# Optimization experiments

Measured on AMD Instinct MI355X. Metric: run time of the kernel, lower is better.

The kernel has to match this reference:

```python
import jax, jax.numpy as jnp
import numpy as np
from jax import lax

# config: B=8, T=32, input_chans=1, H=kernel_size=8, W=n_freq=256
# F1=32, F2=48, F3=256, F4=128, n_note=88, pooling_size=2, filter_size3=(3,64)
B, T, CIN, H, W = 8, 32, 1, 8, 256
F1, F2, F3, F4, NNOTE = 32, 48, 256, 128, 88


def _conv2d(x, w, b, padding):
    # x: (B, Cin, H, W), w: (Cout, Cin, kh, kw)
    y = lax.conv_general_dilated(x, w, (1, 1), padding,
                                 dimension_numbers=('NCHW', 'OIHW', 'NCHW'))
    return y + b[None, :, None, None]


def _clstm(x, w, b, F):
    # x: (B, C, T, H, W); ConvLSTM (no peephole, no LN), 'same' padding.
    xs = jnp.moveaxis(x, 2, 0)  # (T, B, C, H, W)
    h0 = jnp.zeros((x.shape[0], F, x.shape[3], x.shape[4]), x.dtype)
    c0 = h0

    def step(carry, xt):
        h, c = carry
        z = _conv2d(jnp.concatenate([xt, h], axis=1), w, b, 'SAME')
        i, f, g, o = jnp.split(z, 4, axis=1)
        c = jax.nn.sigmoid(f) * c + jax.nn.sigmoid(i) * jnp.tanh(g)
        h = jax.nn.sigmoid(o) * jnp.tanh(c)
        return (h, c), h

    _, hs = lax.scan(step, (h0, c0), xs)  # (T, B, F, H, W)
    return jnp.moveaxis(hs, 0, 2)  # (B, F, T, H, W)


def _maxpool3d(x):
    # MaxPool3d(kernel=2, stride=2) over (T, H, W) of a (B, C, T, H, W) tensor
    return lax.reduce_window(x, -jnp.inf, lax.max,
                             (1, 1, 2, 2, 2), (1, 1, 2, 2, 2), 'VALID')


def setup_inputs() -> dict:
    key = jax.random.key(0)
    ks = jax.random.split(key, 11)
    s = 0.05
    return {
        'x':  jax.random.normal(ks[0], (B, CIN, T, H, W), jnp.float32),
        'w1': jax.random.normal(ks[1], (4 * F1, CIN + F1, 3, 3), jnp.float32) * s,
        'b1': jnp.zeros((4 * F1,), jnp.float32),
        'w2': jax.random.normal(ks[2], (4 * F2, F1 + F2, 3, 3), jnp.float32) * s,
        'b2': jnp.zeros((4 * F2,), jnp.float32),
        'w3': jax.random.normal(ks[3], (F3, F2, 3, 64), jnp.float32) * s,
        'b3': jnp.zeros((F3,), jnp.float32),
        'w4': jax.random.normal(ks[4], (F4, F3, 1, 1), jnp.float32) * s,
        'b4': jnp.zeros((F4,), jnp.float32),
        'w5': jax.random.normal(ks[5], (NNOTE, F4, 1, 1), jnp.float32) * s,
        'b5': jnp.zeros((NNOTE,), jnp.float32),
    }


def reference(x, w1, b1, w2, b2, w3, b3, w4, b4, w5, b5):
    x = _clstm(x, w1, b1, F1)          # (B, F1, T, H, W)
    x = _maxpool3d(x)                  # (B, F1, T/2, H/2, W/2)
    x = _clstm(x, w2, b2, F2)          # (B, F2, T/2, H/2, W/2)
    x = _maxpool3d(x)                  # (B, F2, 8, 2, 64)
    x = x.reshape(B, F2, -1, 64)       # (B, F2, 16, 64), filter_size3[1]=64
    x = jax.nn.elu(_conv2d(x, w3, b3, 'VALID'))  # (B, F3, 14, 1); dropout=eval noop
    x = jax.nn.elu(_conv2d(x, w4, b4, 'VALID'))  # (B, F4, 14, 1)
    x = _conv2d(x, w5, b5, 'VALID')              # (B, 88, 14, 1)
    return x
```

## Files before the change

kernel.cpp:

```cpp
#include <hip/hip_runtime.h>
#include <math.h>


#define DEVINL static __device__ __forceinline__
typedef __attribute__((ext_vector_type(8))) short short8;
typedef __attribute__((ext_vector_type(4))) float f32x4;

#define PLANE_W3 2359296

DEVINL float sigm(float x) { return 1.0f / (1.0f + __expf(-x)); }
DEVINL float tanh_fast(float x) { return 1.0f - 2.0f / (__expf(2.0f * x) + 1.0f); }
DEVINL float elu(float x) { return x > 0.0f ? x : expm1f(x); }
DEVINL unsigned short bf16_rne(float v) {
    unsigned u = __float_as_uint(v);
    unsigned r = (u + 0x7FFF + ((u >> 16) & 1)) >> 16;
    return (unsigned short)r;
}
DEVINL float bf16_to_f(unsigned short h) { return __uint_as_float(((unsigned)h) << 16); }
DEVINL unsigned pack_hl(float v) {
    unsigned short hi = bf16_rne(v);
    unsigned short lo = bf16_rne(v - bf16_to_f(hi));
    return (unsigned)hi | ((unsigned)lo << 16);
}
DEVINL float upk(unsigned u) {
    return __uint_as_float(u << 16) + __uint_as_float(u & 0xffff0000u);
}

DEVINL void lstm1_body(
    int xq, int y, int b, int t,
    const unsigned* __restrict__ xpk, const unsigned short* __restrict__ w1F,
    const float* __restrict__ b1,
    const unsigned* __restrict__ hprev, const unsigned* __restrict__ hpool,
    unsigned* __restrict__ hout, float* __restrict__ c1,
    unsigned* __restrict__ p1pk)
{
    __shared__ __align__(16) unsigned short sBhi[34 * 128];
    __shared__ __align__(16) unsigned short sBlo[34 * 128];
    const int x0 = xq * 32;
    const int tid = threadIdx.x;

    if (((t & 1) == 0) && t >= 2 && (y & 1) == 1) {
        int tp = (t >> 1) - 1, yp = y >> 1;
        for (int e = tid; e < 512; e += 256) {
            int f = e >> 4, xl = e & 15;
            int xp = (x0 >> 1) + xl, gx = x0 + 2 * xl;
            int b0 = ((b * 32 + f) * 8 + (y - 1)) * 256 + gx;
            float m = upk(hpool[b0]);
            m = fmaxf(m, upk(hpool[b0 + 1]));
            m = fmaxf(m, upk(hpool[b0 + 256]));
            m = fmaxf(m, upk(hpool[b0 + 257]));
            m = fmaxf(m, upk(hprev[b0]));
            m = fmaxf(m, upk(hprev[b0 + 1]));
            m = fmaxf(m, upk(hprev[b0 + 256]));
            m = fmaxf(m, upk(hprev[b0 + 257]));
            p1pk[(((b * 32 + f) * 16 + tp) * 4 + yp) * 128 + xp] = pack_hl(m);
        }
    }

    for (int e = tid; e < 34 * 128; e += 256) {
        int lx = e % 34, kk = e / 34;
        unsigned u = 0;
        if (kk < 99) {
            int ci = kk / 3, dy = kk - ci * 3;
            int gy = y + dy - 1, gx = x0 + lx - 1;
            if (gy >= 0 && gy < 8 && gx >= 0 && gx < 256)
                u = (ci == 0) ? xpk[((b * 32 + t) * 8 + gy) * 256 + gx]
                              : hprev[((b * 32 + (ci - 1)) * 8 + gy) * 256 + gx];
        }
        int a16 = lx * 128 + (((kk >> 3) ^ (lx & 15)) << 3) + (kk & 7);
        sBhi[a16] = (unsigned short)u;
        sBlo[a16] = (unsigned short)(u >> 16);
    }
    __syncthreads();

    const int l = tid & 63;
    const int wv = __builtin_amdgcn_readfirstlane(tid >> 6);
    const int ln = l & 15, kg = l >> 4;
    f32x4 acc[2][2];
#pragma unroll
    for (int i = 0; i < 2; ++i)
#pragma unroll
        for (int j = 0; j < 2; ++j) acc[i][j] = (f32x4){0.f, 0.f, 0.f, 0.f};

#pragma unroll
    for (int kk = 0; kk < 4; ++kk) {
        short8 bh[2][3], bl[2][3];
#pragma unroll
        for (int ntl = 0; ntl < 2; ++ntl)
#pragma unroll
            for (int dx = 0; dx < 3; ++dx) {
                int lx = ntl * 16 + ln + dx;
                int slot = kk * 4 + kg;
                int boff = lx * 128 + ((slot ^ (lx & 15)) << 3);
                bh[ntl][dx] = *(const short8*)&sBhi[boff];
                bl[ntl][dx] = *(const short8*)&sBlo[boff];
            }
#pragma unroll
        for (int mtl = 0; mtl < 2; ++mtl)
#pragma unroll
            for (int dx = 0; dx < 3; ++dx) {
                int aoff = ((((dx * 8 + wv * 2 + mtl) * 4 + kk) * 4 + kg) * 16 + ln) * 8;
                short8 ah = *(const short8*)&w1F[aoff];
#pragma unroll
                for (int ntl = 0; ntl < 2; ++ntl) {
                    acc[mtl][ntl] = __builtin_amdgcn_mfma_f32_16x16x32_bf16(ah, bl[ntl][dx], acc[mtl][ntl], 0, 0, 0);
                    acc[mtl][ntl] = __builtin_amdgcn_mfma_f32_16x16x32_bf16(ah, bh[ntl][dx], acc[mtl][ntl], 0, 0, 0);
                }
            }
    }

#pragma unroll
    for (int mtl = 0; mtl < 2; ++mtl) {
        const int f = (wv * 2 + mtl) * 4 + kg;
        const float bi = b1[f], bff = b1[32 + f], bg = b1[64 + f], bo = b1[96 + f];
#pragma unroll
        for (int ntl = 0; ntl < 2; ++ntl) {
            f32x4 a = acc[mtl][ntl];
            int gidx = ((b * 32 + f) * 8 + y) * 256 + x0 + ntl * 16 + ln;
            float zi = a[0] + bi, zf = a[1] + bff, zg = a[2] + bg, zo = a[3] + bo;
            float cv = c1[gidx];
            float cn = sigm(zf) * cv + sigm(zi) * tanh_fast(zg);
            c1[gidx] = cn;
            hout[gidx] = pack_hl(sigm(zo) * tanh_fast(cn));
        }
    }
}

DEVINL void lstm2_body(
    int xq, int y, int b, int t,
    const unsigned* __restrict__ p1pk, const unsigned short* __restrict__ w2F,
    const float* __restrict__ b2,
    const unsigned* __restrict__ hprev, const unsigned* __restrict__ hpool,
    float* __restrict__ c2, unsigned* __restrict__ hout,
    unsigned short* __restrict__ p2hi, unsigned short* __restrict__ p2lo)
{
    __shared__ __align__(16) unsigned short sChi[18 * 256];
    __shared__ __align__(16) unsigned short sClo[18 * 256];
    const int x0 = xq * 16;
    const int tid = threadIdx.x;

    if (((t & 1) == 0) && t >= 2 && y < 2) {
        int tp = (t >> 1) - 1;
        for (int e = tid; e < 48 * 8; e += 256) {
            int f = e >> 3, xl = e & 7;
            int xp = xq * 8 + xl;
            int g0 = ((b * 48 + f) * 4 + y * 2) * 128 + xp * 2;
            float m = fmaxf(fmaxf(upk(hpool[g0]), upk(hpool[g0 + 1])),
                            fmaxf(upk(hpool[g0 + 128]), upk(hpool[g0 + 129])));
            m = fmaxf(m, fmaxf(fmaxf(upk(hprev[g0]), upk(hprev[g0 + 1])),
                               fmaxf(upk(hprev[g0 + 128]), upk(hprev[g0 + 129]))));
            int pi = ((b * 48 + f) * 16 + tp * 2 + y) * 64 + xp;
            unsigned pm = pack_hl(m);
            p2hi[pi] = (unsigned short)pm;
            p2lo[pi] = (unsigned short)(pm >> 16);
        }
    }

    for (int idx = tid; idx < 80 * 54; idx += 256) {
        int ci = idx / 54, rem = idx % 54;
        int dy = rem / 18, lx = rem % 18;
        int gy = y + dy - 1, gx = x0 + lx - 1;
        unsigned u = 0;
        if (gy >= 0 && gy < 4 && gx >= 0 && gx < 128)
            u = (ci < 32) ? p1pk[(((b * 32 + ci) * 16 + t) * 4 + gy) * 128 + gx]
                          : hprev[((b * 48 + (ci - 32)) * 4 + gy) * 128 + gx];
        int k = ci * 3 + dy;
        int a16 = lx * 256 + (((k >> 3) ^ (lx & 15)) << 3) + (k & 7);
        sChi[a16] = (unsigned short)u;
        sClo[a16] = (unsigned short)(u >> 16);
    }
    for (int e = tid; e < 18 * 16; e += 256) {
        int lx = e >> 4, k = 240 + (e & 15);
        int a16 = lx * 256 + (((k >> 3) ^ (lx & 15)) << 3) + (k & 7);
        sChi[a16] = 0;
        sClo[a16] = 0;
    }
    __syncthreads();

    const int l = tid & 63;
    const int wv = __builtin_amdgcn_readfirstlane(tid >> 6);
    const int ln = l & 15, kg = l >> 4;
    f32x4 acc[3] = {{0.f,0.f,0.f,0.f},{0.f,0.f,0.f,0.f},{0.f,0.f,0.f,0.f}};

#pragma unroll
    for (int kk = 0; kk < 8; ++kk) {
        short8 bh[3], bl[3];
#pragma unroll
        for (int dx = 0; dx < 3; ++dx) {
            int lx = ln + dx;
            int boff = lx * 256 + ((((kk << 2) + kg) ^ (lx & 15)) << 3);
            bh[dx] = *(const short8*)&sChi[boff];
            bl[dx] = *(const short8*)&sClo[boff];
        }
#pragma unroll
        for (int j = 0; j < 3; ++j) {
            int mt = wv * 3 + j;
#pragma unroll
            for (int dx = 0; dx < 3; ++dx) {
                int aoff = ((((dx * 12 + mt) * 8 + kk) * 4 + kg) * 16 + ln) * 8;
                short8 ah = *(const short8*)&w2F[aoff];
                acc[j] = __builtin_amdgcn_mfma_f32_16x16x32_bf16(ah, bl[dx], acc[j], 0, 0, 0);
                acc[j] = __builtin_amdgcn_mfma_f32_16x16x32_bf16(ah, bh[dx], acc[j], 0, 0, 0);
            }
        }
    }

    const int x = x0 + ln;
#pragma unroll
    for (int j = 0; j < 3; ++j) {
        int mt = wv * 3 + j;
        int f = mt * 4 + kg;
        float zi = acc[j][0] + b2[f];
        float zf = acc[j][1] + b2[48 + f];
        float zg = acc[j][2] + b2[96 + f];
        float zo = acc[j][3] + b2[144 + f];
        int gidx = ((b * 48 + f) * 4 + y) * 128 + x;
        float cv = c2[gidx];
        float cn = sigm(zf) * cv + sigm(zi) * tanh_fast(zg);
        c2[gidx] = cn;
        hout[gidx] = pack_hl(sigm(zo) * tanh_fast(cn));
    }
}

__global__ __launch_bounds__(256) void step_k(
    const unsigned* __restrict__ xpk, const unsigned short* __restrict__ w1F,
    const float* __restrict__ b1,
    const unsigned* __restrict__ hprev1, const unsigned* __restrict__ hpool1,
    unsigned* __restrict__ hout1, float* __restrict__ c1,
    unsigned* __restrict__ p1pk,
    const unsigned short* __restrict__ w2F, const float* __restrict__ b2,
    const unsigned* __restrict__ hprev2, const unsigned* __restrict__ hpool2,
    unsigned* __restrict__ hout2, float* __restrict__ c2,
    unsigned short* __restrict__ p2hi, unsigned short* __restrict__ p2lo,
    int t, int t2)
{
    int bid = blockIdx.x;
    if (gridDim.x == 768) {
        if (bid < 256) {
            lstm2_body(bid & 7, (bid >> 3) & 3, bid >> 5, t2,
                       p1pk, w2F, b2, hprev2, hpool2, c2, hout2, p2hi, p2lo);
            return;
        }
        bid -= 256;
    }
    lstm1_body(bid & 7, (bid >> 3) & 7, bid >> 6, t,
               xpk, w1F, b1, hprev1, hpool1, hout1, c1, p1pk);
}

__global__ __launch_bounds__(256) void lstm2_k(
    const unsigned* __restrict__ p1pk, const unsigned short* __restrict__ w2F,
    const float* __restrict__ b2,
    const unsigned* __restrict__ hprev, const unsigned* __restrict__ hpool,
    float* __restrict__ c2, unsigned* __restrict__ hout,
    unsigned short* __restrict__ p2hi, unsigned short* __restrict__ p2lo, int t)
{
    int bid = blockIdx.x;
    lstm2_body(bid & 7, (bid >> 3) & 3, bid >> 5, t,
               p1pk, w2F, b2, hprev, hpool, c2, hout, p2hi, p2lo);
}

__global__ void pool1k(const unsigned* __restrict__ hA, const unsigned* __restrict__ hB,
                       unsigned* __restrict__ p1pk, int tp)
{
    int idx = blockIdx.x * 256 + threadIdx.x;
    if (idx >= 8 * 32 * 4 * 128) return;
    int xp = idx & 127, t1 = idx >> 7;
    int yp = t1 & 3, t2 = t1 >> 2;
    int f = t2 & 31, b = t2 >> 5;
    int base = ((b * 32 + f) * 8 + yp * 2) * 256 + xp * 2;
    float m = upk(hA[base]);
    m = fmaxf(m, upk(hA[base + 1]));
    m = fmaxf(m, upk(hA[base + 256]));
    m = fmaxf(m, upk(hA[base + 257]));
    m = fmaxf(m, upk(hB[base]));
    m = fmaxf(m, upk(hB[base + 1]));
    m = fmaxf(m, upk(hB[base + 256]));
    m = fmaxf(m, upk(hB[base + 257]));
    p1pk[(((b * 32 + f) * 16 + tp) * 4 + yp) * 128 + xp] = pack_hl(m);
}

__global__ void pool2(const unsigned* __restrict__ hA, const unsigned* __restrict__ hB,
                      unsigned short* __restrict__ p2hi, unsigned short* __restrict__ p2lo,
                      int tp)
{
    int idx = blockIdx.x * 256 + threadIdx.x;
    if (idx >= 8 * 48 * 2 * 64) return;
    int xp = idx & 63;
    int t1 = idx >> 6;
    int yp = t1 & 1; t1 >>= 1;
    int f = t1 % 48, b = t1 / 48;
    float m = -INFINITY;
#pragma unroll
    for (int dy = 0; dy < 2; ++dy)
#pragma unroll
        for (int dx = 0; dx < 2; ++dx) {
            int g = ((b * 48 + f) * 4 + yp * 2 + dy) * 128 + xp * 2 + dx;
            m = fmaxf(m, fmaxf(upk(hA[g]), upk(hB[g])));
        }
    int pi = ((b * 48 + f) * 16 + tp * 2 + yp) * 64 + xp;
    unsigned pm = pack_hl(m);
    p2hi[pi] = (unsigned short)pm;
    p2lo[pi] = (unsigned short)(pm >> 16);
}

__global__ __launch_bounds__(256) void conv3_part(
    const unsigned short* __restrict__ p2hi, const unsigned short* __restrict__ p2lo,
    const unsigned short* __restrict__ w3F,
    float* __restrict__ part)
{
    __shared__ float sRed[4 * 7 * 256];
    const int mq = blockIdx.x, ck = blockIdx.y;
    const int tid = threadIdx.x;
    const int l = tid & 63;
    const int wv = __builtin_amdgcn_readfirstlane(tid >> 6);
    const int c = ck * 4 + wv;
    const int ln = l & 15, kg = l >> 4;

    int rowbase[7];
#pragma unroll
    for (int nt = 0; nt < 7; ++nt) {
        int col = nt * 16 + ln;
        int bi = col / 14, r = col % 14;
        rowbase[nt] = (bi * 48 + c) * 16 + r;
    }

    f32x4 acc[7];
#pragma unroll
    for (int nt = 0; nt < 7; ++nt) acc[nt] = (f32x4){0.f, 0.f, 0.f, 0.f};

#pragma unroll
    for (int kk = 0; kk < 6; ++kk) {
        int aoff = ((((mq * 48 + c) * 6 + kk) * 4 + kg) * 16 + ln) * 8;
        short8 ah = *(const short8*)&w3F[aoff];
        short8 al = *(const short8*)&w3F[PLANE_W3 + aoff];
        int s = kk * 4 + kg;
        int dr = s >> 3, w0 = (s & 7) * 8;
#pragma unroll
        for (int nt = 0; nt < 7; ++nt) {
            int boff = (rowbase[nt] + dr) * 64 + w0;
            short8 bh = *(const short8*)&p2hi[boff];
            short8 bl = *(const short8*)&p2lo[boff];
            acc[nt] = __builtin_amdgcn_mfma_f32_16x16x32_bf16(al, bh, acc[nt], 0, 0, 0);
            acc[nt] = __builtin_amdgcn_mfma_f32_16x16x32_bf16(ah, bl, acc[nt], 0, 0, 0);
            acc[nt] = __builtin_amdgcn_mfma_f32_16x16x32_bf16(ah, bh, acc[nt], 0, 0, 0);
        }
    }

#pragma unroll
    for (int nt = 0; nt < 7; ++nt)
        *(f32x4*)&sRed[wv * 1792 + nt * 256 + l * 4] = acc[nt];
    __syncthreads();

#pragma unroll
    for (int nt = 0; nt < 7; ++nt) {
        float s = sRed[nt * 256 + tid] + sRed[1792 + nt * 256 + tid] +
                  sRed[2 * 1792 + nt * 256 + tid] + sRed[3 * 1792 + nt * 256 + tid];
        int r16 = (tid >> 6) * 4 + (tid & 3);
        int m = mq * 16 + r16;
        int col = nt * 16 + ((tid >> 2) & 15);
        part[(ck * 256 + m) * 112 + col] = s;
    }
}

__global__ __launch_bounds__(256) void head(
    const float* __restrict__ part, const float* __restrict__ b3,
    const float* __restrict__ w4T, const float* __restrict__ b4,
    const float* __restrict__ w5T, const float* __restrict__ b5,
    float* __restrict__ out)
{
    __shared__ float sO3[256];
    __shared__ float sO4[128];
    const int col = blockIdx.x;
    const int b = col / 14, r = col % 14;
    const int tid = threadIdx.x;

    float s = b3[tid];
#pragma unroll
    for (int ck = 0; ck < 12; ++ck)
        s += part[(ck * 256 + tid) * 112 + col];
    sO3[tid] = elu(s);
    __syncthreads();

    if (tid < 128) {
        float a4 = b4[tid];
        for (int c = 0; c < 256; ++c)
            a4 = fmaf(sO3[c], w4T[c * 128 + tid], a4);
        sO4[tid] = elu(a4);
    }
    __syncthreads();

    if (tid < 88) {
        float a5 = b5[tid];
        for (int c = 0; c < 128; ++c)
            a5 = fmaf(sO4[c], w5T[c * 88 + tid], a5);
        out[(b * 88 + tid) * 14 + r] = a5;
    }
}

__global__ void prep(const float* __restrict__ x, const float* __restrict__ w1,
                     const float* __restrict__ w2, const float* __restrict__ w3,
                     const float* __restrict__ w4, const float* __restrict__ w5,
                     unsigned* __restrict__ zeroA,
                     unsigned* __restrict__ zeroB,
                     unsigned* __restrict__ xpk,
                     unsigned short* __restrict__ w1F, unsigned short* __restrict__ w2F,
                     unsigned short* __restrict__ w3F,
                     float* __restrict__ w4T, float* __restrict__ w5T)
{
    int i = blockIdx.x * 256 + threadIdx.x;
    if (i < 65536) {
        uint4 z = {0, 0, 0, 0};
        uint4* p = (uint4*)&zeroA[i * 16];
        p[0] = z; p[1] = z; p[2] = z; p[3] = z;
        return;
    }
    i -= 65536;
    if (i < 24576) {
        uint4 z = {0, 0, 0, 0};
        uint4* p = (uint4*)&zeroB[i * 16];
        p[0] = z; p[1] = z; p[2] = z; p[3] = z;
        return;
    }
    i -= 24576;
    if (i < 131072) {
        const float4 v = *(const float4*)&x[i * 4];
        uint4 o;
        o.x = pack_hl(v.x); o.y = pack_hl(v.y);
        o.z = pack_hl(v.z); o.w = pack_hl(v.w);
        *(uint4*)&xpk[i * 4] = o;
        return;
    }
    i -= 131072;
    if (i < 6144) {
        int base = i * 8;
        int dx = base / 16384, rem = base % 16384;
        int mt = rem / 2048, r2 = rem % 2048;
        int kk = r2 / 512, r3 = r2 % 512;
        int kg = r3 / 128, ln = (r3 % 128) / 8;
        int f = mt * 4 + (ln >> 2), gate = ln & 3;
        int co = gate * 32 + f;
        int k0 = kk * 32 + kg * 8;
        short8 h;
#pragma unroll
        for (int e = 0; e < 8; ++e) {
            int k = k0 + e;
            float v = (k < 99) ? w1[co * 297 + (k / 3) * 9 + (k % 3) * 3 + dx] : 0.0f;
            h[e] = (short)bf16_rne(v);
        }
        *(short8*)&w1F[base] = h;
        return;
    }
    i -= 6144;
    if (i < 18432) {
        int base = i * 8;
        int dx = base / 49152, rem = base % 49152;
        int mt = rem / 4096, r2 = rem % 4096;
        int kk = r2 / 512, r3 = r2 % 512;
        int kg = r3 / 128, ln = (r3 % 128) / 8;
        int f = mt * 4 + (ln >> 2), gate = ln & 3;
        int co = gate * 48 + f;
        int k0 = kk * 32 + kg * 8;
        short8 h;
#pragma unroll
        for (int e = 0; e < 8; ++e) {
            int k = k0 + e;
            float v = (k < 240) ? w2[co * 720 + (k / 3) * 9 + (k % 3) * 3 + dx] : 0.0f;
            h[e] = (short)bf16_rne(v);
        }
        *(short8*)&w2F[base] = h;
        return;
    }
    i -= 18432;
    if (i < 294912) {
        int base = i * 8;
        int mq = base / 147456, rem = base % 147456;
        int c = rem / 3072, r2 = rem % 3072;
        int kk = r2 / 512, r3 = r2 % 512;
        int kg = r3 / 128, ln = (r3 % 128) / 8;
        int m = mq * 16 + ln;
        int kc0 = kk * 32 + kg * 8;
        int dr = kc0 >> 6, w0 = kc0 & 63;
        const float* src = &w3[((m * 48 + c) * 3 + dr) * 64 + w0];
        short8 hh, hl;
#pragma unroll
        for (int e = 0; e < 8; ++e) {
            float v = src[e];
            unsigned short hi = bf16_rne(v);
            hh[e] = (short)hi;
            hl[e] = (short)bf16_rne(v - bf16_to_f(hi));
        }
        *(short8*)&w3F[base] = hh;
        *(short8*)&w3F[PLANE_W3 + base] = hl;
        return;
    }
    i -= 294912;
    if (i < 32768) {
        int n = i / 256, cch = i % 256;
        w4T[cch * 128 + n] = w4[i];
        return;
    }
    i -= 32768;
    if (i < 11264) {
        int n = i / 128, cch = i % 128;
        w5T[cch * 88 + n] = w5[i];
    }
}

extern "C" void kernel_launch(void* const* d_in, const int* in_sizes, int n_in,
                              void* d_out, int out_size, void* d_ws, size_t ws_size,
                              hipStream_t stream)
{
    const float* x  = (const float*)d_in[0];
    const float* w1 = (const float*)d_in[1];
    const float* b1 = (const float*)d_in[2];
    const float* w2 = (const float*)d_in[3];
    const float* b2 = (const float*)d_in[4];
    const float* w3 = (const float*)d_in[5];
    const float* b3 = (const float*)d_in[6];
    const float* w4 = (const float*)d_in[7];
    const float* b4 = (const float*)d_in[8];
    const float* w5 = (const float*)d_in[9];
    const float* b5 = (const float*)d_in[10];
    float* out = (float*)d_out;

    float* ws = (float*)d_ws;
    size_t off = 0;
    auto alloc = [&](size_t n) { float* p = ws + off; off += n; return p; };
    unsigned* h1[3];
    h1[0] = (unsigned*)alloc(524288); h1[1] = (unsigned*)alloc(524288);
    h1[2] = (unsigned*)alloc(524288);
    float* c1 = alloc(524288);
    unsigned* xpk = (unsigned*)alloc(524288);
    unsigned* p1pk = (unsigned*)alloc(2097152);
    unsigned* h2[3];
    h2[0] = (unsigned*)alloc(196608); h2[1] = (unsigned*)alloc(196608);
    h2[2] = (unsigned*)alloc(196608);
    float* c2 = alloc(196608);
    unsigned short* p2hi = (unsigned short*)alloc(196608);
    unsigned short* p2lo = (unsigned short*)alloc(196608);
    float* part = alloc(344064);
    unsigned short* w1F = (unsigned short*)alloc(24576);
    unsigned short* w2F = (unsigned short*)alloc(73728);
    unsigned short* w3F = (unsigned short*)alloc(2359296);
    float* w4T = alloc(32768);
    float* w5T = alloc(11264);
    (void)ws_size; (void)off;

    prep<<<2284, 256, 0, stream>>>(x, w1, w2, w3, w4, w5,
                                   h1[2], h2[2], xpk, w1F, w2F, w3F, w4T, w5T);

    for (int t = 0; t < 32; ++t) {
        int t2 = ((t & 1) == 0 && t >= 4) ? (t - 4) / 2 : (t == 31 ? 14 : -1);
        int nblk = (t2 >= 0) ? 768 : 512;
        step_k<<<nblk, 256, 0, stream>>>(
            xpk, w1F, b1, h1[(t + 2) % 3], h1[(t + 1) % 3], h1[t % 3], c1, p1pk,
            w2F, b2,
            t2 >= 0 ? h2[(t2 + 2) % 3] : h2[0],
            t2 >= 0 ? h2[(t2 + 1) % 3] : h2[0],
            t2 >= 0 ? h2[t2 % 3] : h2[0],
            c2, p2hi, p2lo, t, t2);
    }
    pool1k<<<512, 256, 0, stream>>>(h1[0], h1[1], p1pk, 15);

    lstm2_k<<<256, 256, 0, stream>>>(p1pk, w2F, b2, h2[2], h2[1], c2, h2[0],
                                     p2hi, p2lo, 15);
    pool2<<<192, 256, 0, stream>>>(h2[2], h2[0], p2hi, p2lo, 7);

    conv3_part<<<dim3(16, 12), 256, 0, stream>>>(p2hi, p2lo, w3F, part);
    head<<<112, 256, 0, stream>>>(part, b3, w4T, b4, w5T, b5, out);
}
```

Measured before the change: 484.2 us.

## Fuse two LSTM1 timesteps per launch with halo recompute and in-kernel pooling

Each launch now computes two consecutive ConvLSTM1 timesteps per block. The first step is evaluated over a halo-extended tile, so the second step can read h from LDS instead of global memory. This halves the step-kernel launch count from 32 to 16 and fuses the 3D max-pool into the second step's epilogue. It also drops the separate pool1k kernel and the h1 zeroing in prep. The cost is redundant halo computation (extra MFMA work on the first step), more registers for 8x2 accumulators, and a large LDS footprint that may reduce occupancy.

```diff
diff --git a/kernel.cpp b/kernel.cpp
--- a/kernel.cpp
+++ b/kernel.cpp
@@ -26,116 +26,15 @@
     return __uint_as_float(u << 16) + __uint_as_float(u & 0xffff0000u);
 }
 
-DEVINL void lstm1_body(
-    int xq, int y, int b, int t,
-    const unsigned* __restrict__ xpk, const unsigned short* __restrict__ w1F,
-    const float* __restrict__ b1,
-    const unsigned* __restrict__ hprev, const unsigned* __restrict__ hpool,
-    unsigned* __restrict__ hout, float* __restrict__ c1,
-    unsigned* __restrict__ p1pk)
-{
-    __shared__ __align__(16) unsigned short sBhi[34 * 128];
-    __shared__ __align__(16) unsigned short sBlo[34 * 128];
-    const int x0 = xq * 32;
-    const int tid = threadIdx.x;
-
-    if (((t & 1) == 0) && t >= 2 && (y & 1) == 1) {
-        int tp = (t >> 1) - 1, yp = y >> 1;
-        for (int e = tid; e < 512; e += 256) {
-            int f = e >> 4, xl = e & 15;
-            int xp = (x0 >> 1) + xl, gx = x0 + 2 * xl;
-            int b0 = ((b * 32 + f) * 8 + (y - 1)) * 256 + gx;
-            float m = upk(hpool[b0]);
-            m = fmaxf(m, upk(hpool[b0 + 1]));
-            m = fmaxf(m, upk(hpool[b0 + 256]));
-            m = fmaxf(m, upk(hpool[b0 + 257]));
-            m = fmaxf(m, upk(hprev[b0]));
-            m = fmaxf(m, upk(hprev[b0 + 1]));
-            m = fmaxf(m, upk(hprev[b0 + 256]));
-            m = fmaxf(m, upk(hprev[b0 + 257]));
-            p1pk[(((b * 32 + f) * 16 + tp) * 4 + yp) * 128 + xp] = pack_hl(m);
-        }
-    }
-
-    for (int e = tid; e < 34 * 128; e += 256) {
-        int lx = e % 34, kk = e / 34;
-        unsigned u = 0;
-        if (kk < 99) {
-            int ci = kk / 3, dy = kk - ci * 3;
-            int gy = y + dy - 1, gx = x0 + lx - 1;
-            if (gy >= 0 && gy < 8 && gx >= 0 && gx < 256)
-                u = (ci == 0) ? xpk[((b * 32 + t) * 8 + gy) * 256 + gx]
-                              : hprev[((b * 32 + (ci - 1)) * 8 + gy) * 256 + gx];
-        }
-        int a16 = lx * 128 + (((kk >> 3) ^ (lx & 15)) << 3) + (kk & 7);
-        sBhi[a16] = (unsigned short)u;
-        sBlo[a16] = (unsigned short)(u >> 16);
-    }
-    __syncthreads();
-
-    const int l = tid & 63;
-    const int wv = __builtin_amdgcn_readfirstlane(tid >> 6);
-    const int ln = l & 15, kg = l >> 4;
-    f32x4 acc[2][2];
-#pragma unroll
-    for (int i = 0; i < 2; ++i)
-#pragma unroll
-        for (int j = 0; j < 2; ++j) acc[i][j] = (f32x4){0.f, 0.f, 0.f, 0.f};
-
-#pragma unroll
-    for (int kk = 0; kk < 4; ++kk) {
-        short8 bh[2][3], bl[2][3];
-#pragma unroll
-        for (int ntl = 0; ntl < 2; ++ntl)
-#pragma unroll
-            for (int dx = 0; dx < 3; ++dx) {
-                int lx = ntl * 16 + ln + dx;
-                int slot = kk * 4 + kg;
-                int boff = lx * 128 + ((slot ^ (lx & 15)) << 3);
-                bh[ntl][dx] = *(const short8*)&sBhi[boff];
-                bl[ntl][dx] = *(const short8*)&sBlo[boff];
-            }
-#pragma unroll
-        for (int mtl = 0; mtl < 2; ++mtl)
-#pragma unroll
-            for (int dx = 0; dx < 3; ++dx) {
-                int aoff = ((((dx * 8 + wv * 2 + mtl) * 4 + kk) * 4 + kg) * 16 + ln) * 8;
-                short8 ah = *(const short8*)&w1F[aoff];
-#pragma unroll
-                for (int ntl = 0; ntl < 2; ++ntl) {
-                    acc[mtl][ntl] = __builtin_amdgcn_mfma_f32_16x16x32_bf16(ah, bl[ntl][dx], acc[mtl][ntl], 0, 0, 0);
-                    acc[mtl][ntl] = __builtin_amdgcn_mfma_f32_16x16x32_bf16(ah, bh[ntl][dx], acc[mtl][ntl], 0, 0, 0);
-                }
-            }
-    }
-
-#pragma unroll
-    for (int mtl = 0; mtl < 2; ++mtl) {
-        const int f = (wv * 2 + mtl) * 4 + kg;
-        const float bi = b1[f], bff = b1[32 + f], bg = b1[64 + f], bo = b1[96 + f];
-#pragma unroll
-        for (int ntl = 0; ntl < 2; ++ntl) {
-            f32x4 a = acc[mtl][ntl];
-            int gidx = ((b * 32 + f) * 8 + y) * 256 + x0 + ntl * 16 + ln;
-            float zi = a[0] + bi, zf = a[1] + bff, zg = a[2] + bg, zo = a[3] + bo;
-            float cv = c1[gidx];
-            float cn = sigm(zf) * cv + sigm(zi) * tanh_fast(zg);
-            c1[gidx] = cn;
-            hout[gidx] = pack_hl(sigm(zo) * tanh_fast(cn));
-        }
-    }
-}
-
 DEVINL void lstm2_body(
     int xq, int y, int b, int t,
     const unsigned* __restrict__ p1pk, const unsigned short* __restrict__ w2F,
     const float* __restrict__ b2,
     const unsigned* __restrict__ hprev, const unsigned* __restrict__ hpool,
     float* __restrict__ c2, unsigned* __restrict__ hout,
-    unsigned short* __restrict__ p2hi, unsigned short* __restrict__ p2lo)
-{
-    __shared__ __align__(16) unsigned short sChi[18 * 256];
-    __shared__ __align__(16) unsigned short sClo[18 * 256];
+    unsigned short* __restrict__ p2hi, unsigned short* __restrict__ p2lo,
+    unsigned short* sChi, unsigned short* sClo)
+{
     const int x0 = xq * 16;
     const int tid = threadIdx.x;
 
@@ -222,29 +121,181 @@
     }
 }
 
-__global__ __launch_bounds__(256) void step_k(
-    const unsigned* __restrict__ xpk, const unsigned short* __restrict__ w1F,
+__global__ __launch_bounds__(256) void fused_k(
+    const unsigned* __restrict__ xpk,
+    const unsigned short* __restrict__ w1F,
     const float* __restrict__ b1,
-    const unsigned* __restrict__ hprev1, const unsigned* __restrict__ hpool1,
-    unsigned* __restrict__ hout1, float* __restrict__ c1,
+    const unsigned* __restrict__ h1prev,
+    unsigned* __restrict__ h1out,
+    const float* __restrict__ cPrev,
+    float* __restrict__ cOut,
     unsigned* __restrict__ p1pk,
     const unsigned short* __restrict__ w2F, const float* __restrict__ b2,
     const unsigned* __restrict__ hprev2, const unsigned* __restrict__ hpool2,
     unsigned* __restrict__ hout2, float* __restrict__ c2,
     unsigned short* __restrict__ p2hi, unsigned short* __restrict__ p2lo,
-    int t, int t2)
-{
+    int j, int t2)
+{
+    __shared__ __align__(16) unsigned char lds[59392];
+    unsigned short* sBhi = (unsigned short*)lds;
+    unsigned short* sBlo = sBhi + 12288;
+    unsigned* hRaw = (unsigned*)(lds + 49152);
+
     int bid = blockIdx.x;
-    if (gridDim.x == 768) {
+    if (gridDim.x == 512) {
         if (bid < 256) {
             lstm2_body(bid & 7, (bid >> 3) & 3, bid >> 5, t2,
-                       p1pk, w2F, b2, hprev2, hpool2, c2, hout2, p2hi, p2lo);
+                       p1pk, w2F, b2, hprev2, hpool2, c2, hout2, p2hi, p2lo,
+                       sBhi, sBhi + 4608);
             return;
         }
         bid -= 256;
     }
-    lstm1_body(bid & 7, (bid >> 3) & 7, bid >> 6, t,
-               xpk, w1F, b1, hprev1, hpool1, hout1, c1, p1pk);
+    const int xq = bid & 31, b = bid >> 5;
+    const int X0 = xq * 8;
+    const int t0 = 2 * j;
+    const int tid = threadIdx.x;
+    const int l = tid & 63;
+    const int w = __builtin_amdgcn_readfirstlane(tid >> 6);
+    const int ln = l & 15, kg = l >> 4;
+    const int row = 2 * w + (ln >> 3);
+
+    for (int e = tid; e < 12288; e += 256) ((unsigned*)sBhi)[e] = 0;
+    __syncthreads();
+
+    for (int e = tid; e < 9504; e += 256) {
+        int k = e % 99, pc = e / 99;
+        int r = pc / 12, tc = pc % 12;
+        int ci = k / 3, dy = k - ci * 3;
+        int gy = r + dy - 1, gx = X0 + tc - 2;
+        unsigned u = 0;
+        if (gy >= 0 && gy < 8 && gx >= 0 && gx < 256)
+            u = (ci == 0) ? xpk[((b * 32 + t0) * 8 + gy) * 256 + gx]
+                          : (j ? h1prev[((b * 32 + ci - 1) * 8 + gy) * 256 + gx] : 0u);
+        int a16 = pc * 128 + (((k >> 3) ^ (pc & 15)) << 3) + (k & 7);
+        sBhi[a16] = (unsigned short)u;
+        sBlo[a16] = (unsigned short)(u >> 16);
+    }
+    __syncthreads();
+
+    f32x4 acc[8][2];
+#pragma unroll
+    for (int mt = 0; mt < 8; ++mt) {
+        acc[mt][0] = (f32x4){0.f, 0.f, 0.f, 0.f};
+        acc[mt][1] = (f32x4){0.f, 0.f, 0.f, 0.f};
+    }
+#pragma unroll
+    for (int kk = 0; kk < 4; ++kk) {
+#pragma unroll
+        for (int dx = 0; dx < 3; ++dx) {
+            short8 bh[2], bl[2];
+#pragma unroll
+            for (int cc = 0; cc < 2; ++cc) {
+                int col = cc * 8 + (ln & 7) - 1;
+                int pc = row * 12 + col + dx + 1;
+                int boff = pc * 128 + (((kk * 4 + kg) ^ (pc & 15)) << 3);
+                bh[cc] = *(const short8*)&sBhi[boff];
+                bl[cc] = *(const short8*)&sBlo[boff];
+            }
+#pragma unroll
+            for (int mt = 0; mt < 8; ++mt) {
+                int aoff = ((((dx * 8 + mt) * 4 + kk) * 4 + kg) * 16 + ln) * 8;
+                short8 ah = *(const short8*)&w1F[aoff];
+#pragma unroll
+                for (int cc = 0; cc < 2; ++cc) {
+                    acc[mt][cc] = __builtin_amdgcn_mfma_f32_16x16x32_bf16(ah, bl[cc], acc[mt][cc], 0, 0, 0);
+                    acc[mt][cc] = __builtin_amdgcn_mfma_f32_16x16x32_bf16(ah, bh[cc], acc[mt][cc], 0, 0, 0);
+                }
+            }
+        }
+    }
+
+    float cA[8][2];
+#pragma unroll
+    for (int mt = 0; mt < 8; ++mt) {
+        const int f = mt * 4 + kg;
+        const float bi = b1[f], bff = b1[32 + f], bg = b1[64 + f], bo = b1[96 + f];
+#pragma unroll
+        for (int cc = 0; cc < 2; ++cc) {
+            int col = cc * 8 + (ln & 7) - 1;
+            int gcol = X0 + col;
+            f32x4 a = acc[mt][cc];
+            float zi = a[0] + bi, zf = a[1] + bff, zg = a[2] + bg, zo = a[3] + bo;
+            float cv = 0.0f;
+            if (j > 0 && col <= 8 && gcol >= 0 && gcol < 256)
+                cv = cPrev[((b * 32 + f) * 8 + row) * 256 + gcol];
+            float cn = sigm(zf) * cv + sigm(zi) * tanh_fast(zg);
+            cA[mt][cc] = cn;
+            if (col <= 8)
+                hRaw[((f * 8) + row) * 10 + col + 1] = pack_hl(sigm(zo) * tanh_fast(cn));
+        }
+    }
+    __syncthreads();
+
+    for (int e = tid; e < 7920; e += 256) {
+        int k = e % 99, pc2 = e / 99;
+        int r = pc2 / 10, tc = pc2 % 10 + 1;
+        int ci = k / 3, dy = k - ci * 3;
+        int gy = r + dy - 1, gx = X0 + tc - 2;
+        unsigned u = 0;
+        if (gy >= 0 && gy < 8 && gx >= 0 && gx < 256)
+            u = (ci == 0) ? xpk[((b * 32 + t0 + 1) * 8 + gy) * 256 + gx]
+                          : hRaw[((ci - 1) * 8 + gy) * 10 + (tc - 1)];
+        int pc = r * 12 + tc;
+        int a16 = pc * 128 + (((k >> 3) ^ (pc & 15)) << 3) + (k & 7);
+        sBhi[a16] = (unsigned short)u;
+        sBlo[a16] = (unsigned short)(u >> 16);
+    }
+    __syncthreads();
+
+    f32x4 acc2[8];
+#pragma unroll
+    for (int mt = 0; mt < 8; ++mt) acc2[mt] = (f32x4){0.f, 0.f, 0.f, 0.f};
+#pragma unroll
+    for (int kk = 0; kk < 4; ++kk) {
+#pragma unroll
+        for (int dx = 0; dx < 3; ++dx) {
+            int pc = row * 12 + (ln & 7) + dx + 1;
+            int boff = pc * 128 + (((kk * 4 + kg) ^ (pc & 15)) << 3);
+            short8 bh = *(const short8*)&sBhi[boff];
+            short8 bl = *(const short8*)&sBlo[boff];
+#pragma unroll
+            for (int mt = 0; mt < 8; ++mt) {
+                int aoff = ((((dx * 8 + mt) * 4 + kk) * 4 + kg) * 16 + ln) * 8;
+                short8 ah = *(const short8*)&w1F[aoff];
+                acc2[mt] = __builtin_amdgcn_mfma_f32_16x16x32_bf16(ah, bl, acc2[mt], 0, 0, 0);
+                acc2[mt] = __builtin_amdgcn_mfma_f32_16x16x32_bf16(ah, bh, acc2[mt], 0, 0, 0);
+            }
+        }
+    }
+
+#pragma unroll
+    for (int mt = 0; mt < 8; ++mt) {
+        const int f = mt * 4 + kg;
+        const float bi = b1[f], bff = b1[32 + f], bg = b1[64 + f], bo = b1[96 + f];
+        float cs0 = __shfl(cA[mt][0], l + 1, 64);
+        float cs1 = __shfl(cA[mt][1], l & 56, 64);
+        float cv = ((ln & 7) == 7) ? cs1 : cs0;
+        f32x4 a = acc2[mt];
+        float zi = a[0] + bi, zf = a[1] + bff, zg = a[2] + bg, zo = a[3] + bo;
+        float cn = sigm(zf) * cv + sigm(zi) * tanh_fast(zg);
+        float hv = sigm(zo) * tanh_fast(cn);
+        int gidx = ((b * 32 + f) * 8 + row) * 256 + X0 + (ln & 7);
+        cOut[gidx] = cn;
+        h1out[gidx] = pack_hl(hv);
+        float m1 = fmaxf(hv, __shfl_xor(hv, 1, 64));
+        float m = fmaxf(m1, __shfl_xor(m1, 8, 64));
+        if ((l & 9) == 0) {
+            int c0 = (ln & 7) + 1;
+            int hb = (f * 8 + 2 * w) * 10;
+            m = fmaxf(m, upk(hRaw[hb + c0]));
+            m = fmaxf(m, upk(hRaw[hb + c0 + 1]));
+            m = fmaxf(m, upk(hRaw[hb + 10 + c0]));
+            m = fmaxf(m, upk(hRaw[hb + 10 + c0 + 1]));
+            int xp = xq * 4 + ((ln & 7) >> 1);
+            p1pk[(((b * 32 + f) * 16 + j) * 4 + w) * 128 + xp] = pack_hl(m);
+        }
+    }
 }
 
 __global__ __launch_bounds__(256) void lstm2_k(
@@ -254,29 +305,11 @@
     float* __restrict__ c2, unsigned* __restrict__ hout,
     unsigned short* __restrict__ p2hi, unsigned short* __restrict__ p2lo, int t)
 {
+    __shared__ __align__(16) unsigned short sChi[18 * 256];
+    __shared__ __align__(16) unsigned short sClo[18 * 256];
     int bid = blockIdx.x;
     lstm2_body(bid & 7, (bid >> 3) & 3, bid >> 5, t,
-               p1pk, w2F, b2, hprev, hpool, c2, hout, p2hi, p2lo);
-}
-
-__global__ void pool1k(const unsigned* __restrict__ hA, const unsigned* __restrict__ hB,
-                       unsigned* __restrict__ p1pk, int tp)
-{
-    int idx = blockIdx.x * 256 + threadIdx.x;
-    if (idx >= 8 * 32 * 4 * 128) return;
-    int xp = idx & 127, t1 = idx >> 7;
-    int yp = t1 & 3, t2 = t1 >> 2;
-    int f = t2 & 31, b = t2 >> 5;
-    int base = ((b * 32 + f) * 8 + yp * 2) * 256 + xp * 2;
-    float m = upk(hA[base]);
-    m = fmaxf(m, upk(hA[base + 1]));
-    m = fmaxf(m, upk(hA[base + 256]));
-    m = fmaxf(m, upk(hA[base + 257]));
-    m = fmaxf(m, upk(hB[base]));
-    m = fmaxf(m, upk(hB[base + 1]));
-    m = fmaxf(m, upk(hB[base + 256]));
-    m = fmaxf(m, upk(hB[base + 257]));
-    p1pk[(((b * 32 + f) * 16 + tp) * 4 + yp) * 128 + xp] = pack_hl(m);
+               p1pk, w2F, b2, hprev, hpool, c2, hout, p2hi, p2lo, sChi, sClo);
 }
 
 __global__ void pool2(const unsigned* __restrict__ hA, const unsigned* __restrict__ hB,
@@ -400,7 +433,6 @@
 __global__ void prep(const float* __restrict__ x, const float* __restrict__ w1,
                      const float* __restrict__ w2, const float* __restrict__ w3,
                      const float* __restrict__ w4, const float* __restrict__ w5,
-                     unsigned* __restrict__ zeroA,
                      unsigned* __restrict__ zeroB,
                      unsigned* __restrict__ xpk,
                      unsigned short* __restrict__ w1F, unsigned short* __restrict__ w2F,
@@ -408,13 +440,6 @@
                      float* __restrict__ w4T, float* __restrict__ w5T)
 {
     int i = blockIdx.x * 256 + threadIdx.x;
-    if (i < 65536) {
-        uint4 z = {0, 0, 0, 0};
-        uint4* p = (uint4*)&zeroA[i * 16];
-        p[0] = z; p[1] = z; p[2] = z; p[3] = z;
-        return;
-    }
-    i -= 65536;
     if (i < 24576) {
         uint4 z = {0, 0, 0, 0};
         uint4* p = (uint4*)&zeroB[i * 16];
@@ -526,10 +551,10 @@
     float* ws = (float*)d_ws;
     size_t off = 0;
     auto alloc = [&](size_t n) { float* p = ws + off; off += n; return p; };
-    unsigned* h1[3];
+    unsigned* h1[2];
     h1[0] = (unsigned*)alloc(524288); h1[1] = (unsigned*)alloc(524288);
-    h1[2] = (unsigned*)alloc(524288);
-    float* c1 = alloc(524288);
+    float* c1[2];
+    c1[0] = alloc(524288); c1[1] = alloc(524288);
     unsigned* xpk = (unsigned*)alloc(524288);
     unsigned* p1pk = (unsigned*)alloc(2097152);
     unsigned* h2[3];
@@ -546,21 +571,20 @@
     float* w5T = alloc(11264);
     (void)ws_size; (void)off;
 
-    prep<<<2284, 256, 0, stream>>>(x, w1, w2, w3, w4, w5,
-                                   h1[2], h2[2], xpk, w1F, w2F, w3F, w4T, w5T);
-
-    for (int t = 0; t < 32; ++t) {
-        int t2 = ((t & 1) == 0 && t >= 4) ? (t - 4) / 2 : (t == 31 ? 14 : -1);
-        int nblk = (t2 >= 0) ? 768 : 512;
-        step_k<<<nblk, 256, 0, stream>>>(
-            xpk, w1F, b1, h1[(t + 2) % 3], h1[(t + 1) % 3], h1[t % 3], c1, p1pk,
-            w2F, b2,
+    prep<<<2028, 256, 0, stream>>>(x, w1, w2, w3, w4, w5,
+                                   h2[2], xpk, w1F, w2F, w3F, w4T, w5T);
+
+    for (int j = 0; j < 16; ++j) {
+        int t2 = j - 1;
+        int nblk = (j >= 1) ? 512 : 256;
+        fused_k<<<nblk, 256, 0, stream>>>(
+            xpk, w1F, b1, h1[(j + 1) & 1], h1[j & 1], c1[(j + 1) & 1], c1[j & 1],
+            p1pk, w2F, b2,
             t2 >= 0 ? h2[(t2 + 2) % 3] : h2[0],
             t2 >= 0 ? h2[(t2 + 1) % 3] : h2[0],
             t2 >= 0 ? h2[t2 % 3] : h2[0],
-            c2, p2hi, p2lo, t, t2);
-    }
-    pool1k<<<512, 256, 0, stream>>>(h1[0], h1[1], p1pk, 15);
+            c2, p2hi, p2lo, j, t2);
+    }
 
     lstm2_k<<<256, 256, 0, stream>>>(p1pk, w2F, b2, h2[2], h2[1], c2, h2[0],
                                      p2hi, p2lo, 15);
```

Result: slower. 993.5 us (+105.2%).
